# Performance work log

Measured on AMD Instinct MI355X. Metric: run time of the kernel, lower is better.

Reference implementation:

```python
import jax, jax.numpy as jnp
import numpy as np

B, T, N = 512, 1024, 50
ROOT_IDX, END_IDX = 0, 1
NEG_INF = -10000.0


def setup_inputs() -> dict:
    key = jax.random.key(0)
    k1, k2, k3, k4 = jax.random.split(key, 4)
    input_features = jax.random.normal(k1, (B, T, N), dtype=jnp.float32)
    # xavier_uniform on [N, N]: bound = sqrt(6 / (N + N))
    bound = float(np.sqrt(6.0 / (N + N)))
    log_transitions = jax.random.uniform(k2, (N, N), minval=-bound, maxval=bound, dtype=jnp.float32)
    log_transitions = log_transitions.at[:, ROOT_IDX].set(NEG_INF)
    log_transitions = log_transitions.at[END_IDX, :].set(NEG_INF)
    target_tags = jax.random.randint(k3, (B, T), 0, N).astype(jnp.int64)
    # contiguous prefix mask from random lengths in [T//2, T]
    lengths = jax.random.randint(k4, (B,), T // 2, T + 1)
    input_mask = (jnp.arange(T)[None, :] < lengths[:, None]).astype(jnp.int32)
    return {
        "input_features": input_features,
        "log_transitions": log_transitions,
        "target_tags": target_tags,
        "input_mask": input_mask,
    }


def _crf_nll(input_features, log_transitions, target_tags, input_mask):
    maskf = input_mask.astype(input_features.dtype)  # [B, T]

    # ---- forward belief propagation (log partition) ----
    alpha0 = log_transitions[ROOT_IDX, :][None, :] + input_features[:, 0, :]  # [B, N]
    feats_t = jnp.swapaxes(input_features, 0, 1)  # [T, B, N]
    mask_t = jnp.swapaxes(maskf, 0, 1)            # [T, B]

    def step(alpha, xs):
        feat, m = xs  # [B, N], [B]
        # next_tag_var[b, i, j] = alpha[b, i] + feat[b, j] + trans[i, j]
        nxt = alpha[:, :, None] + feat[:, None, :] + log_transitions[None, :, :]
        new = jax.nn.logsumexp(nxt, axis=1)  # [B, N]
        m = m[:, None]
        return new * m + alpha * (1.0 - m), None

    alpha, _ = jax.lax.scan(step, alpha0, (feats_t[1:], mask_t[1:]))
    log_z = jax.nn.logsumexp(alpha + log_transitions[:, END_IDX][None, :], axis=-1)  # [B]

    # ---- gold sequence score (vectorized over time) ----
    tags = target_tags  # [B, T]
    scores = log_transitions[ROOT_IDX, tags[:, 0]]  # [B]
    # per-position emission score of the gold tag
    emis = jnp.take_along_axis(input_features, tags[:, :, None], axis=2)[:, :, 0]  # [B, T]
    trans = log_transitions[tags[:, :-1], tags[:, 1:]]  # [B, T-1]
    scores = scores + jnp.sum(trans * maskf[:, 1:], axis=1) + jnp.sum(emis[:, :-1] * maskf[:, :-1], axis=1)
    last_idx = jnp.sum(input_mask, axis=1) - 1  # [B]
    last_tags = jnp.take_along_axis(tags, last_idx[:, None], axis=1)[:, 0]  # [B]
    last_emit = jnp.take_along_axis(input_features[:, -1, :], last_tags[:, None], axis=1)[:, 0]
    scores = scores + log_transitions[last_tags, END_IDX] + last_emit * maskf[:, -1]

    return log_z - scores  # negative log likelihood, [B]


def reference(input_features, log_transitions, target_tags, input_mask):
    return _crf_nll(input_features, log_transitions, target_tags, input_mask)
```

## Files before the change

### kernel.cpp

```cpp
#include <hip/hip_runtime.h>
#include <math.h>

#define BB 512
#define TT 1024
#define NS 50

typedef _Float16 half2_t __attribute__((ext_vector_type(2)));

static __device__ __forceinline__ half2_t pk_h2(float a, float b) {
    auto r = __builtin_amdgcn_cvt_pkrtz(a, b);
    return __builtin_bit_cast(half2_t, r);
}
static __device__ __forceinline__ float wave_sum_f(float v) {
    #pragma unroll
    for (int k = 32; k >= 1; k >>= 1) v += __shfl_xor(v, k, 64);
    return v;
}
static __device__ __forceinline__ int wave_sum_i(int v) {
    #pragma unroll
    for (int k = 32; k >= 1; k >>= 1) v += __shfl_xor(v, k, 64);
    return v;
}
static __device__ __forceinline__ half2_t bcast_h2(half2_t v, int lane) {
    int u = __builtin_amdgcn_readlane(__builtin_bit_cast(int, v), lane);
    return __builtin_bit_cast(half2_t, u);
}
#define FDOT(a, b, c) __builtin_amdgcn_fdot2((a), (b), (c), false)

#define STEP(u, rr, kp, KK, EP, fraw) do {                                   \
    KK += kp;                                                                \
    float p_ = (u) * __int_as_float(rr);                                     \
    int pn_ = __builtin_amdgcn_update_dpp(__float_as_int(p_),                \
                __float_as_int(p_), 0xB1, 0xF, 0xF, true);                   \
    half2_t pp_ = pk_h2(p_, __int_as_float(pn_));                            \
    half2_t b0_ = bcast_h2(pp_, 0),  b1_ = bcast_h2(pp_, 2);                 \
    half2_t b2_ = bcast_h2(pp_, 4),  b3_ = bcast_h2(pp_, 6);                 \
    half2_t b4_ = bcast_h2(pp_, 8),  b5_ = bcast_h2(pp_, 10);                \
    half2_t b6_ = bcast_h2(pp_, 12), b7_ = bcast_h2(pp_, 14);                \
    half2_t b8_ = bcast_h2(pp_, 16), b9_ = bcast_h2(pp_, 18);                \
    half2_t b10_ = bcast_h2(pp_, 20), b11_ = bcast_h2(pp_, 22);              \
    half2_t b12_ = bcast_h2(pp_, 24), b13_ = bcast_h2(pp_, 26);              \
    half2_t b14_ = bcast_h2(pp_, 28), b15_ = bcast_h2(pp_, 30);              \
    half2_t b16_ = bcast_h2(pp_, 32), b17_ = bcast_h2(pp_, 34);              \
    half2_t b18_ = bcast_h2(pp_, 36), b19_ = bcast_h2(pp_, 38);              \
    half2_t b20_ = bcast_h2(pp_, 40), b21_ = bcast_h2(pp_, 42);              \
    half2_t b22_ = bcast_h2(pp_, 44), b23_ = bcast_h2(pp_, 46);              \
    half2_t b24_ = bcast_h2(pp_, 48);                                        \
    float s0_ = 0.f, s1_ = 0.f, s2_ = 0.f, s3_ = 0.f;                        \
    float s4_ = 0.f, s5_ = 0.f, s6_ = 0.f, s7_ = 0.f;                        \
    s0_ = FDOT(b0_,  EP##0,  s0_); s1_ = FDOT(b1_,  EP##1,  s1_);            \
    s2_ = FDOT(b2_,  EP##2,  s2_); s3_ = FDOT(b3_,  EP##3,  s3_);            \
    s4_ = FDOT(b4_,  EP##4,  s4_); s5_ = FDOT(b5_,  EP##5,  s5_);            \
    s6_ = FDOT(b6_,  EP##6,  s6_); s7_ = FDOT(b7_,  EP##7,  s7_);            \
    s0_ = FDOT(b8_,  EP##8,  s0_); s1_ = FDOT(b9_,  EP##9,  s1_);            \
    s2_ = FDOT(b10_, EP##10, s2_); s3_ = FDOT(b11_, EP##11, s3_);            \
    s4_ = FDOT(b12_, EP##12, s4_); s5_ = FDOT(b13_, EP##13, s5_);            \
    s6_ = FDOT(b14_, EP##14, s6_); s7_ = FDOT(b15_, EP##15, s7_);            \
    s0_ = FDOT(b16_, EP##16, s0_); s1_ = FDOT(b17_, EP##17, s1_);            \
    s2_ = FDOT(b18_, EP##18, s2_); s3_ = FDOT(b19_, EP##19, s3_);            \
    s4_ = FDOT(b20_, EP##20, s4_); s5_ = FDOT(b21_, EP##21, s5_);            \
    s6_ = FDOT(b22_, EP##22, s6_); s7_ = FDOT(b23_, EP##23, s7_);            \
    s0_ = FDOT(b24_, EP##24, s0_);                                           \
    float S_ = ((s0_ + s1_) + (s2_ + s3_)) + ((s4_ + s5_) + (s6_ + s7_));    \
    (u) = S_ * __expf(fraw);                                                 \
    int bb_ = __builtin_amdgcn_readlane(__float_as_int(u), 7);               \
    kp = ((bb_ >> 23) & 255) - 127;                                          \
    rr = (127 - kp) << 23;                                                   \
} while (0)

__global__ __launch_bounds__(64, 1) void crf_nll_kernel(
    const float* __restrict__ feat,
    const float* __restrict__ trans,
    const int*   __restrict__ tags,
    const int*   __restrict__ mask,
    float* __restrict__ out)
{
    const int b    = blockIdx.x;
    const int lane = threadIdx.x;
    const int jj   = (lane < NS) ? lane : 0;

#define INIT_EF(m) half2_t ef##m; { \
        float x0 = __expf(trans[(2*(m) + 0) * NS + jj]); \
        float x1 = __expf(trans[(2*(m) + 1) * NS + jj]); \
        if (lane >= NS) { x0 = 0.f; x1 = 0.f; } \
        ef##m = pk_h2(x0, x1); }
#define INIT_EB(m) half2_t eb##m; { \
        float x0 = __expf(trans[jj * NS + 2*(m) + 0]); \
        float x1 = __expf(trans[jj * NS + 2*(m) + 1]); \
        if (lane >= NS) { x0 = 0.f; x1 = 0.f; } \
        eb##m = pk_h2(x0, x1); }
    INIT_EF(0)  INIT_EF(1)  INIT_EF(2)  INIT_EF(3)  INIT_EF(4)
    INIT_EF(5)  INIT_EF(6)  INIT_EF(7)  INIT_EF(8)  INIT_EF(9)
    INIT_EF(10) INIT_EF(11) INIT_EF(12) INIT_EF(13) INIT_EF(14)
    INIT_EF(15) INIT_EF(16) INIT_EF(17) INIT_EF(18) INIT_EF(19)
    INIT_EF(20) INIT_EF(21) INIT_EF(22) INIT_EF(23) INIT_EF(24)
    INIT_EB(0)  INIT_EB(1)  INIT_EB(2)  INIT_EB(3)  INIT_EB(4)
    INIT_EB(5)  INIT_EB(6)  INIT_EB(7)  INIT_EB(8)  INIT_EB(9)
    INIT_EB(10) INIT_EB(11) INIT_EB(12) INIT_EB(13) INIT_EB(14)
    INIT_EB(15) INIT_EB(16) INIT_EB(17) INIT_EB(18) INIT_EB(19)
    INIT_EB(20) INIT_EB(21) INIT_EB(22) INIT_EB(23) INIT_EB(24)
#undef INIT_EF
#undef INIT_EB

    int cnt = 0;
    for (int t = lane; t < TT; t += 64) cnt += mask[b * TT + t];
    const int len = wave_sum_i(cnt);
    const int tm  = (len - 1) >> 1;
    const int nf  = tm;
    const int nb  = len - 1 - tm;

    const float* fb = feat + (size_t)b * TT * NS;

    float uf = (lane < NS) ? __expf(trans[jj] + fb[jj]) : 0.f;
    float ub = (lane < NS) ? __expf(trans[jj * NS + 1] + fb[(size_t)(len - 1) * NS + jj]) : 0.f;
    int Kf = 0, Kb = 0, kpf, kpb, rf, rb;
    { int bb = __builtin_amdgcn_readlane(__float_as_int(uf), 7);
      kpf = ((bb >> 23) & 255) - 127; rf = (127 - kpf) << 23; }
    { int bb = __builtin_amdgcn_readlane(__float_as_int(ub), 7);
      kpb = ((bb >> 23) & 255) - 127; rb = (127 - kpb) << 23; }

    float qf0, qf1, qf2, qf3, qb0, qb1, qb2, qb3;
    {
#define LDF(q, d) { int tl = 1 + (d); tl = (tl < TT) ? tl : TT - 1; q = fb[(size_t)tl * NS + jj]; }
#define LDB(q, d) { int tl = len - 2 - (d); tl = (tl < 0) ? 0 : tl; q = fb[(size_t)tl * NS + jj]; }
        LDF(qf0, 0) LDF(qf1, 1) LDF(qf2, 2) LDF(qf3, 3)
        LDB(qb0, 0) LDB(qb1, 1) LDB(qb2, 2) LDB(qb3, 3)
#undef LDF
#undef LDB
    }

#define PSF(q, d) { float fr_ = q; int tl_ = 1 + k + 4 + (d); \
        tl_ = (tl_ < TT) ? tl_ : TT - 1; q = fb[(size_t)tl_ * NS + jj]; \
        STEP(uf, rf, kpf, Kf, ef, fr_); }
#define PSB(q, d) { float fr_ = q; int tl_ = len - 2 - (k + 4 + (d)); \
        tl_ = (tl_ < 0) ? 0 : tl_; q = fb[(size_t)tl_ * NS + jj]; \
        STEP(ub, rb, kpb, Kb, eb, fr_); }

    int k = 0;
    for (; k + 4 <= nf; k += 4) {
        PSF(qf0, 0) PSB(qb0, 0)
        PSF(qf1, 1) PSB(qb1, 1)
        PSF(qf2, 2) PSB(qb2, 2)
        PSF(qf3, 3) PSB(qb3, 3)
    }
#undef PSF
#undef PSB
    if (k < nf) { STEP(uf, rf, kpf, Kf, ef, qf0); STEP(ub, rb, kpb, Kb, eb, qb0); k++; }
    if (k < nf) { STEP(uf, rf, kpf, Kf, ef, qf1); STEP(ub, rb, kpb, Kb, eb, qb1); k++; }
    if (k < nf) { STEP(uf, rf, kpf, Kf, ef, qf2); STEP(ub, rb, kpb, Kb, eb, qb2); k++; }
    if (nb > nf) {
        float fr = fb[(size_t)(len - 2 - nf) * NS + jj];
        STEP(ub, rb, kpb, Kb, eb, fr);
    }

    float wv = uf * ub * __expf(-fb[(size_t)tm * NS + jj]);
    if (lane >= NS) wv = 0.f;
    float W = wave_sum_f(wv);
    float log_z = __logf(W) + (float)(Kf + Kb) * 0.6931471805599453f;

    const int* tb = tags + (size_t)b * TT;
    float sc = 0.0f;
    for (int t2 = lane; t2 < len; t2 += 64) {
        int tg = tb[t2];
        sc += fb[(size_t)t2 * NS + tg];
        if (t2 >= 1) sc += trans[tb[t2 - 1] * NS + tg];
    }
    sc = wave_sum_f(sc);

    if (lane == 0) {
        sc += trans[tb[0]]
            + trans[tb[len - 1] * NS + 1];
        out[b] = log_z - sc;
    }
}

extern "C" void kernel_launch(void* const* d_in, const int* in_sizes, int n_in,
                              void* d_out, int out_size, void* d_ws, size_t ws_size,
                              hipStream_t stream) {
    const float* feat  = (const float*)d_in[0];
    const float* trans = (const float*)d_in[1];
    const int*   tags  = (const int*)d_in[2];
    const int*   mask  = (const int*)d_in[3];
    float* out = (float*)d_out;
    crf_nll_kernel<<<dim3(BB), dim3(64), 0, stream>>>(feat, trans, tags, mask, out);
}
```

Baseline: 330.3 us.

## Broadcast packed alpha via LDS float4 reads instead of readlane chains

Replaces the 25 scalar readlane broadcasts per step with a write of packed half2 values to shared memory followed by seven float4 LDS reads. The next step's operands are prepared at the end of each step, so the broadcast overlaps with other work. The emission exponentials are now computed when each feature row is prefetched rather than inside the step, which shortens the serial dependency chain. The forward clamp on the prefetch index is dropped, and the lane>=NS zeroing of the final wave sum is removed. Both removals depend on out-of-range values staying harmless, for example zero-padded lanes.

```diff
diff --git a/kernel.cpp b/kernel.cpp
--- a/kernel.cpp
+++ b/kernel.cpp
@@ -21,52 +21,56 @@
     for (int k = 32; k >= 1; k >>= 1) v += __shfl_xor(v, k, 64);
     return v;
 }
-static __device__ __forceinline__ half2_t bcast_h2(half2_t v, int lane) {
-    int u = __builtin_amdgcn_readlane(__builtin_bit_cast(int, v), lane);
-    return __builtin_bit_cast(half2_t, u);
-}
 #define FDOT(a, b, c) __builtin_amdgcn_fdot2((a), (b), (c), false)
+#define H2F(x) __builtin_bit_cast(half2_t, (x))
 
-#define STEP(u, rr, kp, KK, EP, fraw) do {                                   \
-    KK += kp;                                                                \
-    float p_ = (u) * __int_as_float(rr);                                     \
-    int pn_ = __builtin_amdgcn_update_dpp(__float_as_int(p_),                \
-                __float_as_int(p_), 0xB1, 0xF, 0xF, true);                   \
-    half2_t pp_ = pk_h2(p_, __int_as_float(pn_));                            \
-    half2_t b0_ = bcast_h2(pp_, 0),  b1_ = bcast_h2(pp_, 2);                 \
-    half2_t b2_ = bcast_h2(pp_, 4),  b3_ = bcast_h2(pp_, 6);                 \
-    half2_t b4_ = bcast_h2(pp_, 8),  b5_ = bcast_h2(pp_, 10);                \
-    half2_t b6_ = bcast_h2(pp_, 12), b7_ = bcast_h2(pp_, 14);                \
-    half2_t b8_ = bcast_h2(pp_, 16), b9_ = bcast_h2(pp_, 18);                \
-    half2_t b10_ = bcast_h2(pp_, 20), b11_ = bcast_h2(pp_, 22);              \
-    half2_t b12_ = bcast_h2(pp_, 24), b13_ = bcast_h2(pp_, 26);              \
-    half2_t b14_ = bcast_h2(pp_, 28), b15_ = bcast_h2(pp_, 30);              \
-    half2_t b16_ = bcast_h2(pp_, 32), b17_ = bcast_h2(pp_, 34);              \
-    half2_t b18_ = bcast_h2(pp_, 36), b19_ = bcast_h2(pp_, 38);              \
-    half2_t b20_ = bcast_h2(pp_, 40), b21_ = bcast_h2(pp_, 42);              \
-    half2_t b22_ = bcast_h2(pp_, 44), b23_ = bcast_h2(pp_, 46);              \
-    half2_t b24_ = bcast_h2(pp_, 48);                                        \
-    float s0_ = 0.f, s1_ = 0.f, s2_ = 0.f, s3_ = 0.f;                        \
-    float s4_ = 0.f, s5_ = 0.f, s6_ = 0.f, s7_ = 0.f;                        \
-    s0_ = FDOT(b0_,  EP##0,  s0_); s1_ = FDOT(b1_,  EP##1,  s1_);            \
-    s2_ = FDOT(b2_,  EP##2,  s2_); s3_ = FDOT(b3_,  EP##3,  s3_);            \
-    s4_ = FDOT(b4_,  EP##4,  s4_); s5_ = FDOT(b5_,  EP##5,  s5_);            \
-    s6_ = FDOT(b6_,  EP##6,  s6_); s7_ = FDOT(b7_,  EP##7,  s7_);            \
-    s0_ = FDOT(b8_,  EP##8,  s0_); s1_ = FDOT(b9_,  EP##9,  s1_);            \
-    s2_ = FDOT(b10_, EP##10, s2_); s3_ = FDOT(b11_, EP##11, s3_);            \
-    s4_ = FDOT(b12_, EP##12, s4_); s5_ = FDOT(b13_, EP##13, s5_);            \
-    s6_ = FDOT(b14_, EP##14, s6_); s7_ = FDOT(b15_, EP##15, s7_);            \
-    s0_ = FDOT(b16_, EP##16, s0_); s1_ = FDOT(b17_, EP##17, s1_);            \
-    s2_ = FDOT(b18_, EP##18, s2_); s3_ = FDOT(b19_, EP##19, s3_);            \
-    s4_ = FDOT(b20_, EP##20, s4_); s5_ = FDOT(b21_, EP##21, s5_);            \
-    s6_ = FDOT(b22_, EP##22, s6_); s7_ = FDOT(b23_, EP##23, s7_);            \
-    s0_ = FDOT(b24_, EP##24, s0_);                                           \
-    float S_ = ((s0_ + s1_) + (s2_ + s3_)) + ((s4_ + s5_) + (s6_ + s7_));    \
-    (u) = S_ * __expf(fraw);                                                 \
-    int bb_ = __builtin_amdgcn_readlane(__float_as_int(u), 7);               \
-    kp = ((bb_ >> 23) & 255) - 127;                                          \
-    rr = (127 - kp) << 23;                                                   \
+#define HALF(u, rr, kp, K, E, BUF, P0, P1, P2, P3, P4, P5, P6, eexp) do {     \
+    K += kp;                                                                  \
+    float s0_=0.f,s1_=0.f,s2_=0.f,s3_=0.f,s4_=0.f,s5_=0.f,s6_=0.f,s7_=0.f;    \
+    s0_=FDOT(H2F(P0.x),E##0, s0_); s1_=FDOT(H2F(P0.y),E##1, s1_);             \
+    s2_=FDOT(H2F(P0.z),E##2, s2_); s3_=FDOT(H2F(P0.w),E##3, s3_);             \
+    s4_=FDOT(H2F(P1.x),E##4, s4_); s5_=FDOT(H2F(P1.y),E##5, s5_);             \
+    s6_=FDOT(H2F(P1.z),E##6, s6_); s7_=FDOT(H2F(P1.w),E##7, s7_);             \
+    s0_=FDOT(H2F(P2.x),E##8, s0_); s1_=FDOT(H2F(P2.y),E##9, s1_);             \
+    s2_=FDOT(H2F(P2.z),E##10,s2_); s3_=FDOT(H2F(P2.w),E##11,s3_);             \
+    s4_=FDOT(H2F(P3.x),E##12,s4_); s5_=FDOT(H2F(P3.y),E##13,s5_);             \
+    s6_=FDOT(H2F(P3.z),E##14,s6_); s7_=FDOT(H2F(P3.w),E##15,s7_);             \
+    s0_=FDOT(H2F(P4.x),E##16,s0_); s1_=FDOT(H2F(P4.y),E##17,s1_);             \
+    s2_=FDOT(H2F(P4.z),E##18,s2_); s3_=FDOT(H2F(P4.w),E##19,s3_);             \
+    s4_=FDOT(H2F(P5.x),E##20,s4_); s5_=FDOT(H2F(P5.y),E##21,s5_);             \
+    s6_=FDOT(H2F(P5.z),E##22,s6_); s7_=FDOT(H2F(P5.w),E##23,s7_);             \
+    s0_=FDOT(H2F(P6.x),E##24,s0_);                                            \
+    float S_=((s0_+s1_)+(s2_+s3_))+((s4_+s5_)+(s6_+s7_));                     \
+    (u)=S_*(eexp);                                                            \
+    int bb_=__builtin_amdgcn_readlane(__float_as_int(u),7);                   \
+    (kp)=((bb_>>23)&255)-127; (rr)=(127-(kp))<<23;                            \
+    float p_=(u)*__int_as_float(rr);                                          \
+    int pn_=__builtin_amdgcn_update_dpp(__float_as_int(p_),                   \
+              __float_as_int(p_),0xB1,0xF,0xF,true);                          \
+    float pnf_=__int_as_float(pn_);                                           \
+    float lo_=(lane&1)?pnf_:p_, hi_=(lane&1)?p_:pnf_;                         \
+    BUF[lane>>1]=__builtin_bit_cast(float,pk_h2(lo_,hi_));                    \
+    const float4* m4_=(const float4*)(BUF);                                   \
+    P0=m4_[0]; P1=m4_[1]; P2=m4_[2]; P3=m4_[3];                               \
+    P4=m4_[4]; P5=m4_[5]; P6=m4_[6];                                          \
 } while (0)
+
+#define PRIME(u, rr, kp, BUF, P0, P1, P2, P3, P4, P5, P6) do {                \
+    int bb_=__builtin_amdgcn_readlane(__float_as_int(u),7);                   \
+    (kp)=((bb_>>23)&255)-127; (rr)=(127-(kp))<<23;                            \
+    float p_=(u)*__int_as_float(rr);                                          \
+    int pn_=__builtin_amdgcn_update_dpp(__float_as_int(p_),                   \
+              __float_as_int(p_),0xB1,0xF,0xF,true);                          \
+    float pnf_=__int_as_float(pn_);                                           \
+    float lo_=(lane&1)?pnf_:p_, hi_=(lane&1)?p_:pnf_;                         \
+    BUF[lane>>1]=__builtin_bit_cast(float,pk_h2(lo_,hi_));                    \
+    const float4* m4_=(const float4*)(BUF);                                   \
+    P0=m4_[0]; P1=m4_[1]; P2=m4_[2]; P3=m4_[3];                               \
+    P4=m4_[4]; P5=m4_[5]; P6=m4_[6];                                          \
+} while (0)
+
+#define HALF_F(eexp) HALF(uf, rrf, kpf, Kf, ef, bufF, cf0,cf1,cf2,cf3,cf4,cf5,cf6, eexp)
+#define HALF_B(eexp) HALF(ub, rrb, kpb, Kb, eb, bufB, cb0,cb1,cb2,cb3,cb4,cb5,cb6, eexp)
 
 __global__ __launch_bounds__(64, 1) void crf_nll_kernel(
     const float* __restrict__ feat,
@@ -79,16 +83,17 @@
     const int lane = threadIdx.x;
     const int jj   = (lane < NS) ? lane : 0;
 
+    __shared__ __align__(16) float bufF[32];
+    __shared__ __align__(16) float bufB[32];
+
 #define INIT_EF(m) half2_t ef##m; { \
-        float x0 = __expf(trans[(2*(m) + 0) * NS + jj]); \
-        float x1 = __expf(trans[(2*(m) + 1) * NS + jj]); \
-        if (lane >= NS) { x0 = 0.f; x1 = 0.f; } \
-        ef##m = pk_h2(x0, x1); }
+        float x0=__expf(trans[(2*(m)+0)*NS+jj]); \
+        float x1=__expf(trans[(2*(m)+1)*NS+jj]); \
+        if (lane>=NS){x0=0.f;x1=0.f;} ef##m=pk_h2(x0,x1); }
 #define INIT_EB(m) half2_t eb##m; { \
-        float x0 = __expf(trans[jj * NS + 2*(m) + 0]); \
-        float x1 = __expf(trans[jj * NS + 2*(m) + 1]); \
-        if (lane >= NS) { x0 = 0.f; x1 = 0.f; } \
-        eb##m = pk_h2(x0, x1); }
+        float x0=__expf(trans[jj*NS+2*(m)+0]); \
+        float x1=__expf(trans[jj*NS+2*(m)+1]); \
+        if (lane>=NS){x0=0.f;x1=0.f;} eb##m=pk_h2(x0,x1); }
     INIT_EF(0)  INIT_EF(1)  INIT_EF(2)  INIT_EF(3)  INIT_EF(4)
     INIT_EF(5)  INIT_EF(6)  INIT_EF(7)  INIT_EF(8)  INIT_EF(9)
     INIT_EF(10) INIT_EF(11) INIT_EF(12) INIT_EF(13) INIT_EF(14)
@@ -112,49 +117,52 @@
     const float* fb = feat + (size_t)b * TT * NS;
 
     float uf = (lane < NS) ? __expf(trans[jj] + fb[jj]) : 0.f;
-    float ub = (lane < NS) ? __expf(trans[jj * NS + 1] + fb[(size_t)(len - 1) * NS + jj]) : 0.f;
-    int Kf = 0, Kb = 0, kpf, kpb, rf, rb;
-    { int bb = __builtin_amdgcn_readlane(__float_as_int(uf), 7);
-      kpf = ((bb >> 23) & 255) - 127; rf = (127 - kpf) << 23; }
-    { int bb = __builtin_amdgcn_readlane(__float_as_int(ub), 7);
-      kpb = ((bb >> 23) & 255) - 127; rb = (127 - kpb) << 23; }
+    float ub = (lane < NS) ? __expf(trans[jj*NS+1] + fb[(size_t)(len-1)*NS + jj]) : 0.f;
+    int Kf = 0, Kb = 0, kpf, kpb, rrf, rrb;
 
-    float qf0, qf1, qf2, qf3, qb0, qb1, qb2, qb3;
-    {
-#define LDF(q, d) { int tl = 1 + (d); tl = (tl < TT) ? tl : TT - 1; q = fb[(size_t)tl * NS + jj]; }
-#define LDB(q, d) { int tl = len - 2 - (d); tl = (tl < 0) ? 0 : tl; q = fb[(size_t)tl * NS + jj]; }
-        LDF(qf0, 0) LDF(qf1, 1) LDF(qf2, 2) LDF(qf3, 3)
-        LDB(qb0, 0) LDB(qb1, 1) LDB(qb2, 2) LDB(qb3, 3)
-#undef LDF
-#undef LDB
+    float4 cf0, cf1, cf2, cf3, cf4, cf5, cf6;
+    float4 cb0, cb1, cb2, cb3, cb4, cb5, cb6;
+    PRIME(uf, rrf, kpf, bufF, cf0,cf1,cf2,cf3,cf4,cf5,cf6);
+    PRIME(ub, rrb, kpb, bufB, cb0,cb1,cb2,cb3,cb4,cb5,cb6);
+
+    float qf0 = __expf(fb[(size_t)(1)*NS + jj]);
+    float qf1 = __expf(fb[(size_t)(2)*NS + jj]);
+    float qf2 = __expf(fb[(size_t)(3)*NS + jj]);
+    float qf3 = __expf(fb[(size_t)(4)*NS + jj]);
+    float qb0 = __expf(fb[(size_t)(len-2)*NS + jj]);
+    float qb1 = __expf(fb[(size_t)(len-3)*NS + jj]);
+    float qb2 = __expf(fb[(size_t)(len-4)*NS + jj]);
+    float qb3 = __expf(fb[(size_t)(len-5)*NS + jj]);
+
+#define ITER(QF, QB, D) {                                                     \
+        float fx_ = QF;                                                       \
+        { int tl_ = 1 + k + (D) + 4;                                          \
+          QF = __expf(fb[(size_t)tl_ * NS + jj]); }                           \
+        HALF_F(fx_);                                                          \
+        float bx_ = QB;                                                       \
+        { int tl_ = len - 2 - (k + (D) + 4); tl_ = (tl_ < 0) ? 0 : tl_;       \
+          QB = __expf(fb[(size_t)tl_ * NS + jj]); }                           \
+        HALF_B(bx_);                                                          \
     }
-
-#define PSF(q, d) { float fr_ = q; int tl_ = 1 + k + 4 + (d); \
-        tl_ = (tl_ < TT) ? tl_ : TT - 1; q = fb[(size_t)tl_ * NS + jj]; \
-        STEP(uf, rf, kpf, Kf, ef, fr_); }
-#define PSB(q, d) { float fr_ = q; int tl_ = len - 2 - (k + 4 + (d)); \
-        tl_ = (tl_ < 0) ? 0 : tl_; q = fb[(size_t)tl_ * NS + jj]; \
-        STEP(ub, rb, kpb, Kb, eb, fr_); }
 
     int k = 0;
     for (; k + 4 <= nf; k += 4) {
-        PSF(qf0, 0) PSB(qb0, 0)
-        PSF(qf1, 1) PSB(qb1, 1)
-        PSF(qf2, 2) PSB(qb2, 2)
-        PSF(qf3, 3) PSB(qb3, 3)
+        ITER(qf0, qb0, 0)
+        ITER(qf1, qb1, 1)
+        ITER(qf2, qb2, 2)
+        ITER(qf3, qb3, 3)
     }
-#undef PSF
-#undef PSB
-    if (k < nf) { STEP(uf, rf, kpf, Kf, ef, qf0); STEP(ub, rb, kpb, Kb, eb, qb0); k++; }
-    if (k < nf) { STEP(uf, rf, kpf, Kf, ef, qf1); STEP(ub, rb, kpb, Kb, eb, qb1); k++; }
-    if (k < nf) { STEP(uf, rf, kpf, Kf, ef, qf2); STEP(ub, rb, kpb, Kb, eb, qb2); k++; }
+#undef ITER
+    const int d0 = nf - k;
+    if (d0 > 0) { HALF_F(qf0); HALF_B(qb0); }
+    if (d0 > 1) { HALF_F(qf1); HALF_B(qb1); }
+    if (d0 > 2) { HALF_F(qf2); HALF_B(qb2); }
     if (nb > nf) {
-        float fr = fb[(size_t)(len - 2 - nf) * NS + jj];
-        STEP(ub, rb, kpb, Kb, eb, fr);
+        float ee = (d0 == 0) ? qb0 : (d0 == 1) ? qb1 : (d0 == 2) ? qb2 : qb3;
+        HALF_B(ee);
     }
 
     float wv = uf * ub * __expf(-fb[(size_t)tm * NS + jj]);
-    if (lane >= NS) wv = 0.f;
     float W = wave_sum_f(wv);
     float log_z = __logf(W) + (float)(Kf + Kb) * 0.6931471805599453f;
 
```

Result: slower. 346.3 us (+4.9%).
